# Kernel tuning notes

Measured on AMD Instinct MI355X. Metric: run time of the kernel, lower is better.

Reference implementation:

```python
import jax, jax.numpy as jnp
import numpy as np

ALPHA = 0.25        # focal alpha
GAMMA = 2.0         # focal gamma
POS_T = 0.5         # max_iou positive threshold
NEG_T = 0.4         # max_iou negative threshold
SL1_BETA = 1.0 / 9.0  # smooth_l1 with sigma=3
EPS = 1e-6

N, T, A, C = 8, 64, 65536, 80


def setup_inputs() -> dict:
    key = jax.random.key(0)
    ks = jax.random.split(key, 6)
    labels = jax.random.randint(ks[0], (N, T), 1, C)
    y_true = jax.nn.one_hot(labels, C, dtype=jnp.float32)
    xy = jax.random.uniform(ks[1], (N, T, 2)) * 0.7
    wh = jax.random.uniform(ks[2], (N, T, 2)) * 0.25 + 0.02
    bbox_true = jnp.concatenate([xy, xy + wh], axis=-1)
    valid = (jnp.arange(T) < 24).astype(jnp.float32)  # zero-pad remaining GT rows
    bbox_true = bbox_true * valid[None, :, None]
    axy = jax.random.uniform(ks[3], (A, 2)) * 0.9
    awh = jax.random.uniform(jax.random.fold_in(ks[3], 1), (A, 2)) * 0.15 + 0.02
    anchors = jnp.concatenate([axy, axy + awh], axis=-1)
    y_pred = jax.random.normal(ks[4], (N, A, C), dtype=jnp.float32)
    bbox_pred = jax.random.normal(ks[5], (N, A, 4), dtype=jnp.float32) * 0.1
    return {"y_true": y_true, "bbox_true": bbox_true, "y_pred": y_pred,
            "bbox_pred": bbox_pred, "anchors": anchors}


def _iou(b1, b2):
    # b1: (T,4), b2: (A,4) -> (T,A)
    a1 = jnp.maximum(b1[:, 2] - b1[:, 0], 0) * jnp.maximum(b1[:, 3] - b1[:, 1], 0)
    a2 = jnp.maximum(b2[:, 2] - b2[:, 0], 0) * jnp.maximum(b2[:, 3] - b2[:, 1], 0)
    lt = jnp.maximum(b1[:, None, :2], b2[None, :, :2])
    rb = jnp.minimum(b1[:, None, 2:], b2[None, :, 2:])
    wh = jnp.maximum(rb - lt, 0.0)
    inter = wh[..., 0] * wh[..., 1]
    union = a1[:, None] + a2[None, :] - inter
    return inter / jnp.maximum(union, 1e-10)


def _bbox2delta(boxes, anchors):
    # standard (dx, dy, dw, dh) encoding, mean=0 / std=1
    wa = jnp.maximum(anchors[:, 2] - anchors[:, 0], EPS)
    ha = jnp.maximum(anchors[:, 3] - anchors[:, 1], EPS)
    cxa = anchors[:, 0] + 0.5 * wa
    cya = anchors[:, 1] + 0.5 * ha
    wt = jnp.maximum(boxes[:, 2] - boxes[:, 0], EPS)
    ht = jnp.maximum(boxes[:, 3] - boxes[:, 1], EPS)
    cxt = boxes[:, 0] + 0.5 * (boxes[:, 2] - boxes[:, 0])
    cyt = boxes[:, 1] + 0.5 * (boxes[:, 3] - boxes[:, 1])
    return jnp.stack([(cxt - cxa) / wa, (cyt - cya) / ha,
                      jnp.log(wt / wa), jnp.log(ht / ha)], axis=-1)


def _encode_target(y_true_i, bbox_true_i, anchors):
    # y_true_i: (T,C), bbox_true_i: (T,4), anchors: (A,4)
    valid = jnp.any(bbox_true_i > 0, axis=-1)                 # (T,)
    iou = jnp.where(valid[:, None], _iou(bbox_true_i, anchors), -1.0)  # (T,A)
    max_iou = iou.max(axis=0)                                  # (A,)
    assigned = iou.argmax(axis=0)                              # (A,) gt index per anchor
    pos = max_iou >= POS_T
    neg = (max_iou < NEG_T)
    # low-quality matching: each valid gt's best anchor is positive for that gt
    gt_best = iou.argmax(axis=1)                               # (T,)
    gt_best_iou = iou.max(axis=1)
    lq = valid & (gt_best_iou > 0)
    assigned = assigned.at[gt_best].set(jnp.where(lq, jnp.arange(bbox_true_i.shape[0]), assigned[gt_best]))
    pos = pos.at[gt_best].set(jnp.where(lq, True, pos[gt_best]))
    neg = neg & (~pos)
    state = jnp.where(pos, 1, jnp.where(neg, -1, 0)).astype(jnp.int8)[:, None]  # (A,1)
    # class target: background one-hot [1,0,...,0], positives get gt label
    bg = jnp.zeros((anchors.shape[0], y_true_i.shape[-1]), jnp.float32).at[:, 0].set(1.0)
    yt = jnp.where(pos[:, None], y_true_i[assigned], bg)       # (A,C)
    delta = _bbox2delta(bbox_true_i[assigned], anchors)        # (A,4)
    bt = jnp.where(pos[:, None], delta, 0.0)
    return state, yt, bt


def _focal_bce(y_true, logits):
    # elementwise sigmoid focal loss
    ce = jnp.maximum(logits, 0) - logits * y_true + jnp.log1p(jnp.exp(-jnp.abs(logits)))
    p = jax.nn.sigmoid(logits)
    p_t = y_true * p + (1.0 - y_true) * (1.0 - p)
    a_t = y_true * ALPHA + (1.0 - y_true) * (1.0 - ALPHA)
    return a_t * jnp.power(1.0 - p_t, GAMMA) * ce


def _smooth_l1(y_true, y_pred):
    d = jnp.abs(y_true - y_pred)
    return jnp.where(d < SL1_BETA, 0.5 * d * d / SL1_BETA, d - 0.5 * SL1_BETA)


def _sanitize(x):
    return jnp.where(jnp.isnan(x) | jnp.isinf(x), 0.0, x)


def reference(y_true, bbox_true, y_pred, bbox_pred, anchors):
    state, yt, bt = jax.vmap(lambda a, b: _encode_target(a, b, anchors))(y_true, bbox_true)
    positive_w = (state == 1).astype(y_pred.dtype)   # (N,A,1)
    target_w = (state != 0).astype(y_pred.dtype)     # (N,A,1)
    avg_factor = jnp.sum(jnp.maximum(jnp.sum(positive_w, axis=-2), 1.0))
    yt = yt * positive_w                              # background=False zeroes non-positives
    cls = jnp.sum(_focal_bce(yt, y_pred) * target_w) / avg_factor
    box = jnp.sum(_smooth_l1(bt, bbox_pred) * positive_w) / avg_factor
    return _sanitize(cls), _sanitize(box)
```

## Files before the change

kernel.cpp:

```cpp
#include <hip/hip_runtime.h>
#include <hip/hip_bf16.h>
#include <math.h>

#define NB 8
#define TB 64
#define AB 65536
#define CB 80
#define EPSF 1e-6f

#define LOSS_BLOCKS 2048
#define LOSS_ITERS  16

#define WS_CODE_OFF   4096
#define WS_PCLS_OFF   (4096 + NB*AB*4)
#define WS_PBOX_OFF   (WS_PCLS_OFF + LOSS_BLOCKS*4)
#define WS_PPOS_OFF   (WS_PBOX_OFF + LOSS_BLOCKS*4)

__global__ __launch_bounds__(256) void assign_kernel(
    const float* __restrict__ bbox_true,
    const float* __restrict__ anchors,
    int*   __restrict__ code,
    unsigned long long* __restrict__ gt_key)
{
    __shared__ float4 s_box[TB];
    __shared__ float  s_a1[TB];
    __shared__ unsigned long long s_key[TB];

    const int blk   = blockIdx.x;
    const int i     = blk >> 8;
    const int abase = (blk & 255) << 8;
    const int tid   = threadIdx.x;

    if (tid < TB) {
        float4 b = ((const float4*)bbox_true)[i * TB + tid];
        bool valid = (b.x > 0.f) || (b.y > 0.f) || (b.z > 0.f) || (b.w > 0.f);
        float a1 = fmaxf(b.z - b.x, 0.f) * fmaxf(b.w - b.y, 0.f);
        s_box[tid] = b;
        s_a1[tid]  = valid ? a1 : -1.0f;
        s_key[tid] = 0ull;
    }
    __syncthreads();

    const int a = abase + tid;
    const float4 an = ((const float4*)anchors)[a];
    const float a2 = fmaxf(an.z - an.x, 0.f) * fmaxf(an.w - an.y, 0.f);

    float best = -1.0f;
    int bestt = 0;
    #pragma unroll 8
    for (int t = 0; t < TB; ++t) {
        float a1 = s_a1[t];
        float iou = -1.0f;
        if (a1 >= 0.f) {
            float4 b = s_box[t];
            float lx = fmaxf(b.x, an.x), ly = fmaxf(b.y, an.y);
            float rx = fminf(b.z, an.z), ry = fminf(b.w, an.w);
            float w = fmaxf(rx - lx, 0.f), h = fmaxf(ry - ly, 0.f);
            float inter = w * h;
            float uni = a1 + a2 - inter;
            iou = inter / fmaxf(uni, 1e-10f);
            if (iou > 0.f) {
                unsigned long long key =
                    ((unsigned long long)__float_as_uint(iou) << 32) |
                    (unsigned long long)((unsigned)a ^ 0xFFFFFFFFu);
                if (key > s_key[t])
                    atomicMax(&s_key[t], key);
            }
        }
        if (iou > best) { best = iou; bestt = t; }
    }
    bool pos = best >= 0.5f;
    bool neg = best < 0.4f;
    code[i * AB + a] = pos ? bestt : (neg ? -1 : -2);

    __syncthreads();
    if (tid < TB) {
        unsigned long long k = s_key[tid];
        if (k) atomicMax(&gt_key[i * TB + tid], k);
    }
}

__global__ void lq_kernel(const unsigned long long* __restrict__ gt_key,
                          int* __restrict__ code)
{
    __shared__ unsigned long long sk[NB * TB];
    const int tid = threadIdx.x;
    sk[tid] = gt_key[tid];
    __syncthreads();
    const int i = tid >> 6, t = tid & 63;
    unsigned long long k = sk[tid];
    if (k) {
        unsigned a = (unsigned)(k & 0xFFFFFFFFull) ^ 0xFFFFFFFFu;
        bool win = true;
        for (int t2 = t + 1; t2 < TB; ++t2) {
            unsigned long long k2 = sk[(i << 6) | t2];
            if (k2 && (((unsigned)(k2 & 0xFFFFFFFFull) ^ 0xFFFFFFFFu) == a))
                win = false;
        }
        if (win) code[i * AB + (int)a] = t;
    }
}

__device__ __forceinline__ float focal1(bool ypos, float l) {
    float q  = __expf(-fabsf(l));
    float r  = __builtin_amdgcn_rcpf(1.f + q);
    float lg = __logf(r);
    float ce = fmaxf(l, 0.f) - (ypos ? l : 0.f) - lg;
    float p  = (l >= 0.f) ? r : 1.f - r;
    float pt = ypos ? p : 1.f - p;
    float at = ypos ? 0.25f : 0.75f;
    float om = 1.f - pt;
    return at * om * om * ce;
}
__device__ __forceinline__ float smooth_l1(float x) {
    float d = fabsf(x);
    return d < (1.f / 9.f) ? 4.5f * d * d : d - (0.5f / 9.f);
}

__global__ __launch_bounds__(320) void loss_kernel(
    const float* __restrict__ y_true,
    const float* __restrict__ bbox_true,
    const float* __restrict__ y_pred,
    const float* __restrict__ bbox_pred,
    const float* __restrict__ anchors,
    const int*   __restrict__ code,
    float* __restrict__ partial_cls,
    float* __restrict__ partial_box,
    int*   __restrict__ partial_pos)
{
    const int tid   = threadIdx.x;
    const int la    = tid / 20;
    const int chunk = tid % 20;
    const int b   = blockIdx.x;
    const int i   = b >> 8;
    const int sub = b & 255;

    const float4* yp4 = (const float4*)y_pred;
    const float4* yt4 = (const float4*)y_true;

    float cls_acc = 0.f, box_acc = 0.f;
    int posc = 0;

    #pragma unroll 2
    for (int it = 0; it < LOSS_ITERS; ++it) {
        const int a = sub * 16 + la + it * (256 * 16);
        const int g = i * AB + a;
        const int cv = code[g];
        float4 l4 = yp4[g * 20 + chunk];
        if (cv != -2) {
            bool pos = cv >= 0;
            float y0 = 0.f, y1 = 0.f, y2 = 0.f, y3 = 0.f;
            if (pos) {
                float4 yv = yt4[(i * TB + cv) * 20 + chunk];
                y0 = yv.x; y1 = yv.y; y2 = yv.z; y3 = yv.w;
            }
            cls_acc += focal1(y0 != 0.f, l4.x) + focal1(y1 != 0.f, l4.y) +
                       focal1(y2 != 0.f, l4.z) + focal1(y3 != 0.f, l4.w);
            if (pos && chunk == 0) {
                posc += 1;
                float4 bt = ((const float4*)bbox_true)[i * TB + cv];
                float4 an = ((const float4*)anchors)[a];
                float wa = fmaxf(an.z - an.x, EPSF), ha = fmaxf(an.w - an.y, EPSF);
                float cxa = an.x + 0.5f * wa,  cya = an.y + 0.5f * ha;
                float wt = fmaxf(bt.z - bt.x, EPSF), ht = fmaxf(bt.w - bt.y, EPSF);
                float cxt = bt.x + 0.5f * (bt.z - bt.x), cyt = bt.y + 0.5f * (bt.w - bt.y);
                float d0 = (cxt - cxa) / wa, d1 = (cyt - cya) / ha;
                float d2 = __logf(wt / wa),  d3 = __logf(ht / ha);
                float4 bp = ((const float4*)bbox_pred)[g];
                box_acc += smooth_l1(d0 - bp.x) + smooth_l1(d1 - bp.y) +
                           smooth_l1(d2 - bp.z) + smooth_l1(d3 - bp.w);
            }
        }
    }

    for (int off = 32; off > 0; off >>= 1) {
        cls_acc += __shfl_down(cls_acc, off);
        box_acc += __shfl_down(box_acc, off);
        posc    += __shfl_down(posc, off);
    }
    __shared__ float s_cls[5], s_box[5];
    __shared__ int   s_pc[5];
    int wave = tid >> 6, lane = tid & 63;
    if (lane == 0) { s_cls[wave] = cls_acc; s_box[wave] = box_acc; s_pc[wave] = posc; }
    __syncthreads();
    if (tid == 0) {
        partial_cls[b] = s_cls[0] + s_cls[1] + s_cls[2] + s_cls[3] + s_cls[4];
        partial_box[b] = s_box[0] + s_box[1] + s_box[2] + s_box[3] + s_box[4];
        partial_pos[b] = s_pc[0] + s_pc[1] + s_pc[2] + s_pc[3] + s_pc[4];
    }
}

__global__ __launch_bounds__(256) void reduce_kernel(
    const float* __restrict__ partial_cls,
    const float* __restrict__ partial_box,
    const int*   __restrict__ partial_pos,
    float* __restrict__ out)
{
    const int tid = threadIdx.x;
    const int wave = tid >> 6, lane = tid & 63;
    __shared__ double sc[4], sb[4];
    __shared__ int    si[4];
    __shared__ float  s_avg;

    double c = 0.0, bx = 0.0;
    #pragma unroll
    for (int j = 0; j < LOSS_BLOCKS / 256; ++j) {
        c  += (double)partial_cls[tid + j * 256];
        bx += (double)partial_box[tid + j * 256];
    }

    float avg = 0.f;
    for (int bb = 0; bb < NB; ++bb) {
        int p = partial_pos[bb * 256 + tid];
        for (int off = 32; off > 0; off >>= 1) p += __shfl_down(p, off);
        if (lane == 0) si[wave] = p;
        __syncthreads();
        if (tid == 0) {
            int tot = si[0] + si[1] + si[2] + si[3];
            avg += fmaxf((float)tot, 1.0f);
        }
        __syncthreads();
    }
    if (tid == 0) s_avg = avg;

    for (int off = 32; off > 0; off >>= 1) {
        c  += __shfl_down(c, off);
        bx += __shfl_down(bx, off);
    }
    if (lane == 0) { sc[wave] = c; sb[wave] = bx; }
    __syncthreads();
    if (tid == 0) {
        double ct = sc[0] + sc[1] + sc[2] + sc[3];
        double bt = sb[0] + sb[1] + sb[2] + sb[3];
        float cf = (float)(ct / (double)s_avg);
        float bf = (float)(bt / (double)s_avg);
        if (isnan(cf) || isinf(cf)) cf = 0.f;
        if (isnan(bf) || isinf(bf)) bf = 0.f;
        out[0] = cf;
        out[1] = bf;
    }
}

extern "C" void kernel_launch(void* const* d_in, const int* in_sizes, int n_in,
                              void* d_out, int out_size, void* d_ws, size_t ws_size,
                              hipStream_t stream) {
    const float* y_true    = (const float*)d_in[0];
    const float* bbox_true = (const float*)d_in[1];
    const float* y_pred    = (const float*)d_in[2];
    const float* bbox_pred = (const float*)d_in[3];
    const float* anchors   = (const float*)d_in[4];
    float* out = (float*)d_out;

    char* ws = (char*)d_ws;
    unsigned long long* gt_key = (unsigned long long*)ws;
    int*   code        = (int*)(ws + WS_CODE_OFF);
    float* partial_cls = (float*)(ws + WS_PCLS_OFF);
    float* partial_box = (float*)(ws + WS_PBOX_OFF);
    int*   partial_pos = (int*)(ws + WS_PPOS_OFF);

    hipMemsetAsync(ws, 0, NB * TB * sizeof(unsigned long long), stream);

    assign_kernel<<<NB * AB / 256, 256, 0, stream>>>(bbox_true, anchors, code, gt_key);
    lq_kernel<<<1, NB * TB, 0, stream>>>(gt_key, code);
    loss_kernel<<<LOSS_BLOCKS, 320, 0, stream>>>(
        y_true, bbox_true, y_pred, bbox_pred, anchors, code,
        partial_cls, partial_box, partial_pos);
    reduce_kernel<<<1, 256, 0, stream>>>(partial_cls, partial_box, partial_pos, out);
}
```

Measured before the change: 296.5 us.

## Split focal loss into dense all-negative stream plus sparse per-anchor corrections

```diff
diff --git a/kernel.cpp b/kernel.cpp
--- a/kernel.cpp
+++ b/kernel.cpp
@@ -8,13 +8,37 @@
 #define CB 80
 #define EPSF 1e-6f
 
-#define LOSS_BLOCKS 2048
-#define LOSS_ITERS  16
-
-#define WS_CODE_OFF   4096
-#define WS_PCLS_OFF   (4096 + NB*AB*4)
-#define WS_PBOX_OFF   (WS_PCLS_OFF + LOSS_BLOCKS*4)
-#define WS_PPOS_OFF   (WS_PBOX_OFF + LOSS_BLOCKS*4)
+#define WS_POSCNT_OFF 4096
+#define WS_LABEL_OFF  4608
+#define WS_CODE_OFF   8192
+#define WS_PCLS_OFF   (WS_CODE_OFF + NB*AB*4)
+#define WS_PCCLS_OFF  (WS_PCLS_OFF + 4096*4)
+#define WS_PCBOX_OFF  (WS_PCCLS_OFF + 2048*4)
+#define WS_MEMSET_BYTES 4608
+
+__device__ __forceinline__ float focal0(float l) {
+    float q  = __expf(-fabsf(l));
+    float r  = __builtin_amdgcn_rcpf(1.f + q);
+    float lg = __logf(r);
+    float ce = fmaxf(l, 0.f) - lg;
+    float p  = (l >= 0.f) ? r : 1.f - r;
+    return 0.75f * p * p * ce;
+}
+__device__ __forceinline__ float focal_diff(float l) {
+    float q  = __expf(-fabsf(l));
+    float r  = __builtin_amdgcn_rcpf(1.f + q);
+    float lg = __logf(r);
+    float m  = fmaxf(l, 0.f);
+    float p  = (l >= 0.f) ? r : 1.f - r;
+    float f0 = 0.75f * p * p * (m - lg);
+    float om = 1.f - p;
+    float f1 = 0.25f * om * om * (m - l - lg);
+    return f1 - f0;
+}
+__device__ __forceinline__ float smooth_l1(float x) {
+    float d = fabsf(x);
+    return d < (1.f / 9.f) ? 4.5f * d * d : d - (0.5f / 9.f);
+}
 
 __global__ __launch_bounds__(256) void assign_kernel(
     const float* __restrict__ bbox_true,
@@ -33,10 +57,8 @@
 
     if (tid < TB) {
         float4 b = ((const float4*)bbox_true)[i * TB + tid];
-        bool valid = (b.x > 0.f) || (b.y > 0.f) || (b.z > 0.f) || (b.w > 0.f);
-        float a1 = fmaxf(b.z - b.x, 0.f) * fmaxf(b.w - b.y, 0.f);
         s_box[tid] = b;
-        s_a1[tid]  = valid ? a1 : -1.0f;
+        s_a1[tid]  = fmaxf(b.z - b.x, 0.f) * fmaxf(b.w - b.y, 0.f);
         s_key[tid] = 0ull;
     }
     __syncthreads();
@@ -49,23 +71,19 @@
     int bestt = 0;
     #pragma unroll 8
     for (int t = 0; t < TB; ++t) {
-        float a1 = s_a1[t];
-        float iou = -1.0f;
-        if (a1 >= 0.f) {
-            float4 b = s_box[t];
-            float lx = fmaxf(b.x, an.x), ly = fmaxf(b.y, an.y);
-            float rx = fminf(b.z, an.z), ry = fminf(b.w, an.w);
-            float w = fmaxf(rx - lx, 0.f), h = fmaxf(ry - ly, 0.f);
-            float inter = w * h;
-            float uni = a1 + a2 - inter;
-            iou = inter / fmaxf(uni, 1e-10f);
-            if (iou > 0.f) {
-                unsigned long long key =
-                    ((unsigned long long)__float_as_uint(iou) << 32) |
-                    (unsigned long long)((unsigned)a ^ 0xFFFFFFFFu);
-                if (key > s_key[t])
-                    atomicMax(&s_key[t], key);
-            }
+        float4 b = s_box[t];
+        float lx = fmaxf(b.x, an.x), ly = fmaxf(b.y, an.y);
+        float rx = fminf(b.z, an.z), ry = fminf(b.w, an.w);
+        float w = fmaxf(rx - lx, 0.f), h = fmaxf(ry - ly, 0.f);
+        float inter = w * h;
+        float uni = s_a1[t] + a2 - inter;
+        float iou = inter * __builtin_amdgcn_rcpf(fmaxf(uni, 1e-10f));
+        if (iou > 0.f) {
+            unsigned long long key =
+                ((unsigned long long)__float_as_uint(iou) << 32) |
+                (unsigned long long)((unsigned)a ^ 0xFFFFFFFFu);
+            if (key > s_key[t])
+                atomicMax(&s_key[t], key);
         }
         if (iou > best) { best = iou; bestt = t; }
     }
@@ -80,12 +98,21 @@
     }
 }
 
-__global__ void lq_kernel(const unsigned long long* __restrict__ gt_key,
-                          int* __restrict__ code)
+__global__ void lq_label_kernel(const unsigned long long* __restrict__ gt_key,
+                                const float* __restrict__ y_true,
+                                int* __restrict__ code,
+                                int* __restrict__ labels)
 {
     __shared__ unsigned long long sk[NB * TB];
     const int tid = threadIdx.x;
     sk[tid] = gt_key[tid];
+
+    const float* row = y_true + (size_t)tid * CB;
+    int lab = 0;
+    for (int c = 0; c < CB; ++c)
+        if (row[c] > 0.5f) lab = c;
+    labels[tid] = lab;
+
     __syncthreads();
     const int i = tid >> 6, t = tid & 63;
     unsigned long long k = sk[tid];
@@ -101,139 +128,125 @@
     }
 }
 
-__device__ __forceinline__ float focal1(bool ypos, float l) {
-    float q  = __expf(-fabsf(l));
-    float r  = __builtin_amdgcn_rcpf(1.f + q);
-    float lg = __logf(r);
-    float ce = fmaxf(l, 0.f) - (ypos ? l : 0.f) - lg;
-    float p  = (l >= 0.f) ? r : 1.f - r;
-    float pt = ypos ? p : 1.f - p;
-    float at = ypos ? 0.25f : 0.75f;
-    float om = 1.f - pt;
-    return at * om * om * ce;
-}
-__device__ __forceinline__ float smooth_l1(float x) {
-    float d = fabsf(x);
-    return d < (1.f / 9.f) ? 4.5f * d * d : d - (0.5f / 9.f);
-}
-
-__global__ __launch_bounds__(320) void loss_kernel(
-    const float* __restrict__ y_true,
+__global__ __launch_bounds__(256) void stream_kernel(
+    const float4* __restrict__ yp4,
+    float* __restrict__ p_cls)
+{
+    const int tid = threadIdx.x;
+    const int g0  = blockIdx.x * 256 + tid;
+    float acc = 0.f;
+    #pragma unroll
+    for (int j = 0; j < 10; ++j) {
+        float4 v = yp4[g0 + j * 1048576];
+        acc += focal0(v.x) + focal0(v.y) + focal0(v.z) + focal0(v.w);
+    }
+    for (int off = 32; off > 0; off >>= 1) acc += __shfl_down(acc, off);
+    __shared__ float s[4];
+    int wave = tid >> 6, lane = tid & 63;
+    if (lane == 0) s[wave] = acc;
+    __syncthreads();
+    if (tid == 0) p_cls[blockIdx.x] = s[0] + s[1] + s[2] + s[3];
+}
+
+__global__ __launch_bounds__(256) void corr_kernel(
+    const float* __restrict__ y_pred,
     const float* __restrict__ bbox_true,
-    const float* __restrict__ y_pred,
     const float* __restrict__ bbox_pred,
     const float* __restrict__ anchors,
     const int*   __restrict__ code,
-    float* __restrict__ partial_cls,
-    float* __restrict__ partial_box,
-    int*   __restrict__ partial_pos)
-{
-    const int tid   = threadIdx.x;
-    const int la    = tid / 20;
-    const int chunk = tid % 20;
+    const int*   __restrict__ labels,
+    float* __restrict__ p_ccls,
+    float* __restrict__ p_cbox,
+    int*   __restrict__ pos_cnt)
+{
+    const int tid = threadIdx.x;
     const int b   = blockIdx.x;
     const int i   = b >> 8;
-    const int sub = b & 255;
-
-    const float4* yp4 = (const float4*)y_pred;
-    const float4* yt4 = (const float4*)y_true;
-
-    float cls_acc = 0.f, box_acc = 0.f;
+    const int g   = b * 256 + tid;
+    const int a   = g & (AB - 1);
+
+    const int cv = code[g];
+    float cls_c = 0.f, box_c = 0.f;
     int posc = 0;
 
-    #pragma unroll 2
-    for (int it = 0; it < LOSS_ITERS; ++it) {
-        const int a = sub * 16 + la + it * (256 * 16);
-        const int g = i * AB + a;
-        const int cv = code[g];
-        float4 l4 = yp4[g * 20 + chunk];
-        if (cv != -2) {
-            bool pos = cv >= 0;
-            float y0 = 0.f, y1 = 0.f, y2 = 0.f, y3 = 0.f;
-            if (pos) {
-                float4 yv = yt4[(i * TB + cv) * 20 + chunk];
-                y0 = yv.x; y1 = yv.y; y2 = yv.z; y3 = yv.w;
-            }
-            cls_acc += focal1(y0 != 0.f, l4.x) + focal1(y1 != 0.f, l4.y) +
-                       focal1(y2 != 0.f, l4.z) + focal1(y3 != 0.f, l4.w);
-            if (pos && chunk == 0) {
-                posc += 1;
-                float4 bt = ((const float4*)bbox_true)[i * TB + cv];
-                float4 an = ((const float4*)anchors)[a];
-                float wa = fmaxf(an.z - an.x, EPSF), ha = fmaxf(an.w - an.y, EPSF);
-                float cxa = an.x + 0.5f * wa,  cya = an.y + 0.5f * ha;
-                float wt = fmaxf(bt.z - bt.x, EPSF), ht = fmaxf(bt.w - bt.y, EPSF);
-                float cxt = bt.x + 0.5f * (bt.z - bt.x), cyt = bt.y + 0.5f * (bt.w - bt.y);
-                float d0 = (cxt - cxa) / wa, d1 = (cyt - cya) / ha;
-                float d2 = __logf(wt / wa),  d3 = __logf(ht / ha);
-                float4 bp = ((const float4*)bbox_pred)[g];
-                box_acc += smooth_l1(d0 - bp.x) + smooth_l1(d1 - bp.y) +
-                           smooth_l1(d2 - bp.z) + smooth_l1(d3 - bp.w);
-            }
+    if (cv >= 0) {
+        posc = 1;
+        int c = labels[i * TB + cv];
+        float l = y_pred[(size_t)g * CB + c];
+        cls_c = focal_diff(l);
+
+        float4 bt = ((const float4*)bbox_true)[i * TB + cv];
+        float4 an = ((const float4*)anchors)[a];
+        float wa = fmaxf(an.z - an.x, EPSF), ha = fmaxf(an.w - an.y, EPSF);
+        float cxa = an.x + 0.5f * wa,  cya = an.y + 0.5f * ha;
+        float wt = fmaxf(bt.z - bt.x, EPSF), ht = fmaxf(bt.w - bt.y, EPSF);
+        float cxt = bt.x + 0.5f * (bt.z - bt.x), cyt = bt.y + 0.5f * (bt.w - bt.y);
+        float d0 = (cxt - cxa) / wa, d1 = (cyt - cya) / ha;
+        float d2 = __logf(wt / wa),  d3 = __logf(ht / ha);
+        float4 bp = ((const float4*)bbox_pred)[g];
+        box_c = smooth_l1(d0 - bp.x) + smooth_l1(d1 - bp.y) +
+                smooth_l1(d2 - bp.z) + smooth_l1(d3 - bp.w);
+    } else if (cv == -2) {
+        const float4* yp4 = (const float4*)(y_pred + (size_t)g * CB);
+        float s = 0.f;
+        #pragma unroll 4
+        for (int k = 0; k < 20; ++k) {
+            float4 v = yp4[k];
+            s += focal0(v.x) + focal0(v.y) + focal0(v.z) + focal0(v.w);
         }
+        cls_c = -s;
     }
 
     for (int off = 32; off > 0; off >>= 1) {
-        cls_acc += __shfl_down(cls_acc, off);
-        box_acc += __shfl_down(box_acc, off);
-        posc    += __shfl_down(posc, off);
-    }
-    __shared__ float s_cls[5], s_box[5];
-    __shared__ int   s_pc[5];
+        cls_c += __shfl_down(cls_c, off);
+        box_c += __shfl_down(box_c, off);
+        posc  += __shfl_down(posc, off);
+    }
+    __shared__ float sc[4], sb[4];
+    __shared__ int   sp[4];
     int wave = tid >> 6, lane = tid & 63;
-    if (lane == 0) { s_cls[wave] = cls_acc; s_box[wave] = box_acc; s_pc[wave] = posc; }
+    if (lane == 0) { sc[wave] = cls_c; sb[wave] = box_c; sp[wave] = posc; }
     __syncthreads();
     if (tid == 0) {
-        partial_cls[b] = s_cls[0] + s_cls[1] + s_cls[2] + s_cls[3] + s_cls[4];
-        partial_box[b] = s_box[0] + s_box[1] + s_box[2] + s_box[3] + s_box[4];
-        partial_pos[b] = s_pc[0] + s_pc[1] + s_pc[2] + s_pc[3] + s_pc[4];
+        p_ccls[b] = sc[0] + sc[1] + sc[2] + sc[3];
+        p_cbox[b] = sb[0] + sb[1] + sb[2] + sb[3];
+        int p = sp[0] + sp[1] + sp[2] + sp[3];
+        if (p) atomicAdd(&pos_cnt[i], p);
     }
 }
 
 __global__ __launch_bounds__(256) void reduce_kernel(
-    const float* __restrict__ partial_cls,
-    const float* __restrict__ partial_box,
-    const int*   __restrict__ partial_pos,
+    const float* __restrict__ p_cls,
+    const float* __restrict__ p_ccls,
+    const float* __restrict__ p_cbox,
+    const int*   __restrict__ pos_cnt,
     float* __restrict__ out)
 {
     const int tid = threadIdx.x;
     const int wave = tid >> 6, lane = tid & 63;
-    __shared__ double sc[4], sb[4];
-    __shared__ int    si[4];
-    __shared__ float  s_avg;
 
     double c = 0.0, bx = 0.0;
     #pragma unroll
-    for (int j = 0; j < LOSS_BLOCKS / 256; ++j) {
-        c  += (double)partial_cls[tid + j * 256];
-        bx += (double)partial_box[tid + j * 256];
-    }
-
-    float avg = 0.f;
-    for (int bb = 0; bb < NB; ++bb) {
-        int p = partial_pos[bb * 256 + tid];
-        for (int off = 32; off > 0; off >>= 1) p += __shfl_down(p, off);
-        if (lane == 0) si[wave] = p;
-        __syncthreads();
-        if (tid == 0) {
-            int tot = si[0] + si[1] + si[2] + si[3];
-            avg += fmaxf((float)tot, 1.0f);
-        }
-        __syncthreads();
-    }
-    if (tid == 0) s_avg = avg;
+    for (int j = 0; j < 16; ++j) c += (double)p_cls[tid + j * 256];
+    #pragma unroll
+    for (int j = 0; j < 8; ++j)  c += (double)p_ccls[tid + j * 256];
+    #pragma unroll
+    for (int j = 0; j < 8; ++j)  bx += (double)p_cbox[tid + j * 256];
 
     for (int off = 32; off > 0; off >>= 1) {
         c  += __shfl_down(c, off);
         bx += __shfl_down(bx, off);
     }
+    __shared__ double sc[4], sb[4];
     if (lane == 0) { sc[wave] = c; sb[wave] = bx; }
     __syncthreads();
     if (tid == 0) {
+        float avg = 0.f;
+        for (int i = 0; i < NB; ++i) avg += fmaxf((float)pos_cnt[i], 1.0f);
         double ct = sc[0] + sc[1] + sc[2] + sc[3];
         double bt = sb[0] + sb[1] + sb[2] + sb[3];
-        float cf = (float)(ct / (double)s_avg);
-        float bf = (float)(bt / (double)s_avg);
+        float cf = (float)(ct / (double)avg);
+        float bf = (float)(bt / (double)avg);
         if (isnan(cf) || isinf(cf)) cf = 0.f;
         if (isnan(bf) || isinf(bf)) bf = 0.f;
         out[0] = cf;
@@ -253,17 +266,20 @@
 
     char* ws = (char*)d_ws;
     unsigned long long* gt_key = (unsigned long long*)ws;
-    int*   code        = (int*)(ws + WS_CODE_OFF);
-    float* partial_cls = (float*)(ws + WS_PCLS_OFF);
-    float* partial_box = (float*)(ws + WS_PBOX_OFF);
-    int*   partial_pos = (int*)(ws + WS_PPOS_OFF);
-
-    hipMemsetAsync(ws, 0, NB * TB * sizeof(unsigned long long), stream);
+    int*   pos_cnt = (int*)(ws + WS_POSCNT_OFF);
+    int*   labels  = (int*)(ws + WS_LABEL_OFF);
+    int*   code    = (int*)(ws + WS_CODE_OFF);
+    float* p_cls   = (float*)(ws + WS_PCLS_OFF);
+    float* p_ccls  = (float*)(ws + WS_PCCLS_OFF);
+    float* p_cbox  = (float*)(ws + WS_PCBOX_OFF);
+
+    hipMemsetAsync(ws, 0, WS_MEMSET_BYTES, stream);
 
     assign_kernel<<<NB * AB / 256, 256, 0, stream>>>(bbox_true, anchors, code, gt_key);
-    lq_kernel<<<1, NB * TB, 0, stream>>>(gt_key, code);
-    loss_kernel<<<LOSS_BLOCKS, 320, 0, stream>>>(
-        y_true, bbox_true, y_pred, bbox_pred, anchors, code,
-        partial_cls, partial_box, partial_pos);
-    reduce_kernel<<<1, 256, 0, stream>>>(partial_cls, partial_box, partial_pos, out);
-}
+    lq_label_kernel<<<1, NB * TB, 0, stream>>>(gt_key, y_true, code, labels);
+    stream_kernel<<<4096, 256, 0, stream>>>((const float4*)y_pred, p_cls);
+    corr_kernel<<<NB * AB / 256, 256, 0, stream>>>(
+        y_pred, bbox_true, bbox_pred, anchors, code, labels,
+        p_ccls, p_cbox, pos_cnt);
+    reduce_kernel<<<1, 256, 0, stream>>>(p_cls, p_ccls, p_cbox, pos_cnt, out);
+}
```

New measurement: 334.1 us. 12.7% more time.

## Split focal loss into all-negative term plus per-positive label correction

Applied to the files above, without the earlier changes.

```diff
diff --git a/kernel.cpp b/kernel.cpp
--- a/kernel.cpp
+++ b/kernel.cpp
@@ -11,10 +11,32 @@
 #define LOSS_BLOCKS 2048
 #define LOSS_ITERS  16
 
-#define WS_CODE_OFF   4096
-#define WS_PCLS_OFF   (4096 + NB*AB*4)
+#define WS_LABEL_OFF  4096
+#define WS_CODE_OFF   8192
+#define WS_PCLS_OFF   (WS_CODE_OFF + NB*AB*4)
 #define WS_PBOX_OFF   (WS_PCLS_OFF + LOSS_BLOCKS*4)
 #define WS_PPOS_OFF   (WS_PBOX_OFF + LOSS_BLOCKS*4)
+
+__device__ __forceinline__ float focal0(float l) {
+    float u  = __expf(l);
+    float r  = __builtin_amdgcn_rcpf(1.f + u);
+    float p  = 1.f - r;
+    float lg = __log2f(r);
+    return p * p * lg * -0.5198603854f;
+}
+__device__ __forceinline__ float focal_diff(float l) {
+    float u  = __expf(l);
+    float r  = __builtin_amdgcn_rcpf(1.f + u);
+    float p  = 1.f - r;
+    float sp = -0.6931471806f * __log2f(r);
+    float f1 = 0.25f * r * r * (sp - l);
+    float f0 = 0.75f * p * p * sp;
+    return f1 - f0;
+}
+__device__ __forceinline__ float smooth_l1(float x) {
+    float d = fabsf(x);
+    return d < (1.f / 9.f) ? 4.5f * d * d : d - (0.5f / 9.f);
+}
 
 __global__ __launch_bounds__(256) void assign_kernel(
     const float* __restrict__ bbox_true,
@@ -33,10 +55,8 @@
 
     if (tid < TB) {
         float4 b = ((const float4*)bbox_true)[i * TB + tid];
-        bool valid = (b.x > 0.f) || (b.y > 0.f) || (b.z > 0.f) || (b.w > 0.f);
-        float a1 = fmaxf(b.z - b.x, 0.f) * fmaxf(b.w - b.y, 0.f);
         s_box[tid] = b;
-        s_a1[tid]  = valid ? a1 : -1.0f;
+        s_a1[tid]  = fmaxf(b.z - b.x, 0.f) * fmaxf(b.w - b.y, 0.f);
         s_key[tid] = 0ull;
     }
     __syncthreads();
@@ -49,23 +69,19 @@
     int bestt = 0;
     #pragma unroll 8
     for (int t = 0; t < TB; ++t) {
-        float a1 = s_a1[t];
-        float iou = -1.0f;
-        if (a1 >= 0.f) {
-            float4 b = s_box[t];
-            float lx = fmaxf(b.x, an.x), ly = fmaxf(b.y, an.y);
-            float rx = fminf(b.z, an.z), ry = fminf(b.w, an.w);
-            float w = fmaxf(rx - lx, 0.f), h = fmaxf(ry - ly, 0.f);
-            float inter = w * h;
-            float uni = a1 + a2 - inter;
-            iou = inter / fmaxf(uni, 1e-10f);
-            if (iou > 0.f) {
-                unsigned long long key =
-                    ((unsigned long long)__float_as_uint(iou) << 32) |
-                    (unsigned long long)((unsigned)a ^ 0xFFFFFFFFu);
-                if (key > s_key[t])
-                    atomicMax(&s_key[t], key);
-            }
+        float4 b = s_box[t];
+        float lx = fmaxf(b.x, an.x), ly = fmaxf(b.y, an.y);
+        float rx = fminf(b.z, an.z), ry = fminf(b.w, an.w);
+        float w = fmaxf(rx - lx, 0.f), h = fmaxf(ry - ly, 0.f);
+        float inter = w * h;
+        float uni = s_a1[t] + a2 - inter;
+        float iou = inter * __builtin_amdgcn_rcpf(fmaxf(uni, 1e-10f));
+        if (iou > 0.f) {
+            unsigned long long key =
+                ((unsigned long long)__float_as_uint(iou) << 32) |
+                (unsigned long long)((unsigned)a ^ 0xFFFFFFFFu);
+            if (key > s_key[t])
+                atomicMax(&s_key[t], key);
         }
         if (iou > best) { best = iou; bestt = t; }
     }
@@ -80,12 +96,21 @@
     }
 }
 
-__global__ void lq_kernel(const unsigned long long* __restrict__ gt_key,
-                          int* __restrict__ code)
+__global__ void lq_label_kernel(const unsigned long long* __restrict__ gt_key,
+                                const float* __restrict__ y_true,
+                                int* __restrict__ code,
+                                int* __restrict__ labels)
 {
     __shared__ unsigned long long sk[NB * TB];
     const int tid = threadIdx.x;
     sk[tid] = gt_key[tid];
+
+    const float* row = y_true + (size_t)tid * CB;
+    int lab = 0;
+    for (int c = 0; c < CB; ++c)
+        if (row[c] > 0.5f) lab = c;
+    labels[tid] = lab;
+
     __syncthreads();
     const int i = tid >> 6, t = tid & 63;
     unsigned long long k = sk[tid];
@@ -101,29 +126,13 @@
     }
 }
 
-__device__ __forceinline__ float focal1(bool ypos, float l) {
-    float q  = __expf(-fabsf(l));
-    float r  = __builtin_amdgcn_rcpf(1.f + q);
-    float lg = __logf(r);
-    float ce = fmaxf(l, 0.f) - (ypos ? l : 0.f) - lg;
-    float p  = (l >= 0.f) ? r : 1.f - r;
-    float pt = ypos ? p : 1.f - p;
-    float at = ypos ? 0.25f : 0.75f;
-    float om = 1.f - pt;
-    return at * om * om * ce;
-}
-__device__ __forceinline__ float smooth_l1(float x) {
-    float d = fabsf(x);
-    return d < (1.f / 9.f) ? 4.5f * d * d : d - (0.5f / 9.f);
-}
-
 __global__ __launch_bounds__(320) void loss_kernel(
-    const float* __restrict__ y_true,
     const float* __restrict__ bbox_true,
     const float* __restrict__ y_pred,
     const float* __restrict__ bbox_pred,
     const float* __restrict__ anchors,
     const int*   __restrict__ code,
+    const int*   __restrict__ labels,
     float* __restrict__ partial_cls,
     float* __restrict__ partial_box,
     int*   __restrict__ partial_pos)
@@ -136,7 +145,6 @@
     const int sub = b & 255;
 
     const float4* yp4 = (const float4*)y_pred;
-    const float4* yt4 = (const float4*)y_true;
 
     float cls_acc = 0.f, box_acc = 0.f;
     int posc = 0;
@@ -148,27 +156,30 @@
         const int cv = code[g];
         float4 l4 = yp4[g * 20 + chunk];
         if (cv != -2) {
-            bool pos = cv >= 0;
-            float y0 = 0.f, y1 = 0.f, y2 = 0.f, y3 = 0.f;
-            if (pos) {
-                float4 yv = yt4[(i * TB + cv) * 20 + chunk];
-                y0 = yv.x; y1 = yv.y; y2 = yv.z; y3 = yv.w;
-            }
-            cls_acc += focal1(y0 != 0.f, l4.x) + focal1(y1 != 0.f, l4.y) +
-                       focal1(y2 != 0.f, l4.z) + focal1(y3 != 0.f, l4.w);
-            if (pos && chunk == 0) {
-                posc += 1;
-                float4 bt = ((const float4*)bbox_true)[i * TB + cv];
-                float4 an = ((const float4*)anchors)[a];
-                float wa = fmaxf(an.z - an.x, EPSF), ha = fmaxf(an.w - an.y, EPSF);
-                float cxa = an.x + 0.5f * wa,  cya = an.y + 0.5f * ha;
-                float wt = fmaxf(bt.z - bt.x, EPSF), ht = fmaxf(bt.w - bt.y, EPSF);
-                float cxt = bt.x + 0.5f * (bt.z - bt.x), cyt = bt.y + 0.5f * (bt.w - bt.y);
-                float d0 = (cxt - cxa) / wa, d1 = (cyt - cya) / ha;
-                float d2 = __logf(wt / wa),  d3 = __logf(ht / ha);
-                float4 bp = ((const float4*)bbox_pred)[g];
-                box_acc += smooth_l1(d0 - bp.x) + smooth_l1(d1 - bp.y) +
-                           smooth_l1(d2 - bp.z) + smooth_l1(d3 - bp.w);
+            cls_acc += focal0(l4.x) + focal0(l4.y) + focal0(l4.z) + focal0(l4.w);
+            if (cv >= 0) {
+                int lab = labels[i * TB + cv];
+                if (chunk == (lab >> 2)) {
+                    int e = lab & 3;
+                    float le = (e == 0) ? l4.x : (e == 1) ? l4.y
+                             : (e == 2) ? l4.z : l4.w;
+                    cls_acc += focal_diff(le);
+                }
+                if (chunk == 0) {
+                    posc += 1;
+                    float4 bt = ((const float4*)bbox_true)[i * TB + cv];
+                    float4 an = ((const float4*)anchors)[a];
+                    float wa = fmaxf(an.z - an.x, EPSF), ha = fmaxf(an.w - an.y, EPSF);
+                    float cxa = an.x + 0.5f * wa,  cya = an.y + 0.5f * ha;
+                    float wt = fmaxf(bt.z - bt.x, EPSF), ht = fmaxf(bt.w - bt.y, EPSF);
+                    float cxt = bt.x + 0.5f * (bt.z - bt.x);
+                    float cyt = bt.y + 0.5f * (bt.w - bt.y);
+                    float d0 = (cxt - cxa) / wa, d1 = (cyt - cya) / ha;
+                    float d2 = __logf(wt / wa),  d3 = __logf(ht / ha);
+                    float4 bp = ((const float4*)bbox_pred)[g];
+                    box_acc += smooth_l1(d0 - bp.x) + smooth_l1(d1 - bp.y) +
+                               smooth_l1(d2 - bp.z) + smooth_l1(d3 - bp.w);
+                }
             }
         }
     }
@@ -253,17 +264,18 @@
 
     char* ws = (char*)d_ws;
     unsigned long long* gt_key = (unsigned long long*)ws;
-    int*   code        = (int*)(ws + WS_CODE_OFF);
-    float* partial_cls = (float*)(ws + WS_PCLS_OFF);
-    float* partial_box = (float*)(ws + WS_PBOX_OFF);
-    int*   partial_pos = (int*)(ws + WS_PPOS_OFF);
-
-    hipMemsetAsync(ws, 0, NB * TB * sizeof(unsigned long long), stream);
+    int*   labels  = (int*)(ws + WS_LABEL_OFF);
+    int*   code    = (int*)(ws + WS_CODE_OFF);
+    float* p_cls   = (float*)(ws + WS_PCLS_OFF);
+    float* p_box   = (float*)(ws + WS_PBOX_OFF);
+    int*   p_pos   = (int*)(ws + WS_PPOS_OFF);
+
+    hipMemsetAsync(ws, 0, 4096, stream);
 
     assign_kernel<<<NB * AB / 256, 256, 0, stream>>>(bbox_true, anchors, code, gt_key);
-    lq_kernel<<<1, NB * TB, 0, stream>>>(gt_key, code);
+    lq_label_kernel<<<1, NB * TB, 0, stream>>>(gt_key, y_true, code, labels);
     loss_kernel<<<LOSS_BLOCKS, 320, 0, stream>>>(
-        y_true, bbox_true, y_pred, bbox_pred, anchors, code,
-        partial_cls, partial_box, partial_pos);
-    reduce_kernel<<<1, 256, 0, stream>>>(partial_cls, partial_box, partial_pos, out);
-}
+        bbox_true, y_pred, bbox_pred, anchors, code, labels,
+        p_cls, p_box, p_pos);
+    reduce_kernel<<<1, 256, 0, stream>>>(p_cls, p_box, p_pos, out);
+}
```

Result: slower. 308.4 us (+4.0%).
